# Performance work log

Measured on AMD Instinct MI355X. Metric: run time of the kernel, lower is better.

## Reference

```python
import jax, jax.numpy as jnp
import numpy as np
import math

DIM = 4096
N_HEADS = 32
HEAD_DIM = DIM // N_HEADS  # 128
SEQLEN = 2048


def setup_inputs() -> dict:
    key = jax.random.key(0)
    ks = jax.random.split(key, 8)
    x = jax.random.normal(ks[0], (1, SEQLEN, DIM), dtype=jnp.float32)
    # freqs_cis as real view: (seqlen, head_dim//2, 2) = (cos, sin) of rotary angles
    theta = 10000.0 ** (-jnp.arange(0, HEAD_DIM, 2, dtype=jnp.float32) / HEAD_DIM)
    angles = jnp.arange(SEQLEN, dtype=jnp.float32)[:, None] * theta[None, :]
    freqs = jnp.stack([jnp.cos(angles), jnp.sin(angles)], axis=-1)  # (S, 64, 2)
    # causal additive mask (use -1e9 instead of -inf for numeric safety)
    mask = jnp.triu(jnp.full((SEQLEN, SEQLEN), -1e9, dtype=jnp.float32), k=1)[None, None]
    scale = 1.0 / math.sqrt(DIM)
    wq = jax.random.normal(ks[1], (DIM, DIM), dtype=jnp.float32) * scale
    wk = jax.random.normal(ks[2], (DIM, DIM), dtype=jnp.float32) * scale
    wv = jax.random.normal(ks[3], (DIM, DIM), dtype=jnp.float32) * scale
    wo = jax.random.normal(ks[4], (DIM, DIM), dtype=jnp.float32) * scale
    return {"x": x, "start_pos": 0, "freqs": freqs, "mask": mask,
            "wq": wq, "wk": wk, "wv": wv, "wo": wo}


def _rotary(xq, xk, freqs, seqlen, n_heads, head_dim):
    # Faithful to source: note the repo's slice(0, 2) means xq_ == xq (no pair swap).
    ll = freqs[:, :, 0:1]  # (S, hd/2, 1) cos
    rr = freqs[:, :, 1:2]  # (S, hd/2, 1) sin
    fl = jnp.concatenate([ll, ll], axis=-1).reshape(seqlen, 1, head_dim)
    fr = jnp.concatenate([-rr, rr], axis=-1).reshape(seqlen, 1, head_dim)
    xq_ = xq.reshape(seqlen, n_heads, head_dim // 2, 2).reshape(seqlen, n_heads, head_dim)  # == xq
    xk_ = xk.reshape(seqlen, n_heads, head_dim // 2, 2).reshape(seqlen, n_heads, head_dim)  # == xk
    return xq * fl + xq_ * fr, xk * fl + xk_ * fr


def reference(x, start_pos, freqs, mask, wq, wk, wv, wo):
    bsz, seqlen, dim = x.shape  # bsz == 1 (source squeezes batch)
    xs = x[0]  # (S, D) -- HE encrypt/linear/decrypt roundtrip == plain linear
    xq = xs @ wq.T
    xk = xs @ wk.T
    xv = xs @ wv.T
    xq = xq.reshape(seqlen, N_HEADS, HEAD_DIM)
    xk = xk.reshape(seqlen, N_HEADS, HEAD_DIM)
    xv = xv.reshape(seqlen, N_HEADS, HEAD_DIM)
    xq, xk = _rotary(xq, xk, freqs, seqlen, N_HEADS, HEAD_DIM)
    # start_pos == 0 and zero-initialized cache => keys/values are just xk/xv
    q = jnp.transpose(xq, (1, 0, 2))  # (H, S, Dh)
    k = jnp.transpose(xk, (1, 0, 2))
    v = jnp.transpose(xv, (1, 0, 2))
    scores = jnp.einsum('hqd,hkd->hqk', q, k) / math.sqrt(HEAD_DIM)  # (H, S, S)
    scores = scores[None] + mask  # (1, H, S, S)
    probs = jax.nn.softmax(scores, axis=-1)
    out = jnp.einsum('bhqk,hkd->bhqd', probs, v)  # (1, H, S, Dh)
    out = jnp.transpose(out, (0, 2, 1, 3)).reshape(bsz, seqlen, dim)
    return out @ wo.T
```

## Files before the change

kernel.cpp:

```cpp
#include <hip/hip_runtime.h>

#define DIM 4096
#define SEQ 2048
#define NH 32
#define HD 128

typedef __bf16 bf16x8 __attribute__((ext_vector_type(8)));
typedef float f32x4 __attribute__((ext_vector_type(4)));

#define QSCALE 0.12751649736765598f

__device__ inline ushort f2bf(float f) {
    union { float f; unsigned u; } v; v.f = f;
    unsigned r = v.u + 0x7fffu + ((v.u >> 16) & 1u);
    return (ushort)(r >> 16);
}

__global__ void conv_all(const float* __restrict__ x,  const float* __restrict__ wq,
                         const float* __restrict__ wk, const float* __restrict__ wv,
                         const float* __restrict__ wo,
                         ushort* __restrict__ xb,  ushort* __restrict__ wqb,
                         ushort* __restrict__ wkb, ushort* __restrict__ wvb,
                         ushort* __restrict__ wob) {
    int i = blockIdx.x * 256 + threadIdx.x;
    const float* src; ushort* dst; int off;
    const int n4x = (SEQ * DIM) / 4;
    if (i < n4x) { src = x; dst = xb; off = i; }
    else {
        int j = i - n4x;
        int w = j >> 22;
        off = j & ((1 << 22) - 1);
        src = (w == 0) ? wq : (w == 1) ? wk : (w == 2) ? wv : wo;
        dst = (w == 0) ? wqb : (w == 1) ? wkb : (w == 2) ? wvb : wob;
    }
    float4 v = ((const float4*)src)[off];
    ushort4 o;
    o.x = f2bf(v.x); o.y = f2bf(v.y); o.z = f2bf(v.z); o.w = f2bf(v.w);
    ((ushort4*)dst)[off] = o;
}


#define AS1(p) (const __attribute__((address_space(1))) void*)(p)
#define AS3(p) (__attribute__((address_space(3))) void*)(p)
#define FENCE() asm volatile("" ::: "memory")
#define BARRIER() do { FENCE(); __builtin_amdgcn_s_barrier(); FENCE(); } while (0)

__device__ __forceinline__ void gemm256_body(
    const ushort* __restrict__ Ab,
    const ushort* __restrict__ Bb,
    ushort* __restrict__ sA0, ushort* __restrict__ sA1,
    ushort* __restrict__ sB0, ushort* __restrict__ sB1,
    f32x4 acc[8][4], const int ldk, const int klen)
{
    const int tid  = threadIdx.x;
    const int wave = tid >> 6, lane = tid & 63;
    const int quad = lane >> 4, c = lane & 15;
    const int wm = wave >> 2, wn = wave & 3;

    const int aoff  = (lane >> 3) * ldk + (((lane & 7) ^ (lane >> 3)) * 8);
    const int sa_r0 = wave * 8;
    const int sb_r0 = (wave >> 1) * 64 + (wave & 1) * 16;

    const int rp0 = (quad ^ (c & 7)) * 8;
    const int rp1 = ((4 + quad) ^ (c & 7)) * 8;
    const int arow = (wm * 128 + c) * 64;
    const int brow = (wn * 64 + c) * 64;

#define STAGE_A(dst, h, k0) do { \
    const int _r0 = (h) * 64 + sa_r0; \
    __builtin_amdgcn_global_load_lds(AS1(Ab + (size_t)_r0 * ldk + (k0) + aoff), \
                                     AS3((dst) + _r0 * 64), 16, 0, 0); \
    const int _r1 = _r0 + 128; \
    __builtin_amdgcn_global_load_lds(AS1(Ab + (size_t)_r1 * ldk + (k0) + aoff), \
                                     AS3((dst) + _r1 * 64), 16, 0, 0); \
  } while (0)
#define STAGE_B(dst, h, k0) do { \
    const int _r0 = (h) * 32 + sb_r0; \
    __builtin_amdgcn_global_load_lds(AS1(Bb + (size_t)_r0 * ldk + (k0) + aoff), \
                                     AS3((dst) + _r0 * 64), 16, 0, 0); \
    const int _r1 = _r0 + 8; \
    __builtin_amdgcn_global_load_lds(AS1(Bb + (size_t)_r1 * ldk + (k0) + aoff), \
                                     AS3((dst) + _r1 * 64), 16, 0, 0); \
  } while (0)

    bf16x8 af[4][2];
    bf16x8 b0[2][2];
    bf16x8 b1[2][2];

#define READ_AH(buf, mh) do { \
    _Pragma("unroll") \
    for (int _m = 0; _m < 4; ++_m) { \
        af[_m][0] = *(const bf16x8*)&(buf)[arow + (mh) * 4096 + _m * 1024 + rp0]; \
        af[_m][1] = *(const bf16x8*)&(buf)[arow + (mh) * 4096 + _m * 1024 + rp1]; \
    } } while (0)
#define READ_BH(buf, nh, dst) do { \
    _Pragma("unroll") \
    for (int _n = 0; _n < 2; ++_n) { \
        dst[_n][0] = *(const bf16x8*)&(buf)[brow + (nh) * 2048 + _n * 1024 + rp0]; \
        dst[_n][1] = *(const bf16x8*)&(buf)[brow + (nh) * 2048 + _n * 1024 + rp1]; \
    } } while (0)
#define MMA_Q(mh, nq, B) do { \
    __builtin_amdgcn_s_setprio(1); \
    _Pragma("unroll") \
    for (int _kk = 0; _kk < 2; ++_kk) \
    _Pragma("unroll") \
    for (int _m = 0; _m < 4; ++_m) \
    _Pragma("unroll") \
    for (int _n = 0; _n < 2; ++_n) \
        acc[(mh) * 4 + _m][(nq) * 2 + _n] = __builtin_amdgcn_mfma_f32_16x16x32_bf16( \
            af[_m][_kk], B[_n][_kk], acc[(mh) * 4 + _m][(nq) * 2 + _n], 0, 0, 0); \
    __builtin_amdgcn_s_setprio(0); \
  } while (0)

    const int NT = klen >> 6;

    STAGE_B(sB0, 0, 0);  STAGE_A(sA0, 0, 0);
    STAGE_B(sB0, 1, 0);  STAGE_A(sA0, 1, 0);
    STAGE_B(sB1, 0, 64); STAGE_A(sA1, 0, 64);
    STAGE_B(sB1, 1, 64); STAGE_A(sA1, 1, 64);
    asm volatile("s_waitcnt vmcnt(8)" ::: "memory");
    BARRIER();
    READ_BH(sB0, 0, b0);
    BARRIER();

#pragma unroll 1
    for (int t = 0; t < NT; ++t) {
        ushort* cA = (t & 1) ? sA1 : sA0;
        ushort* cB = (t & 1) ? sB1 : sB0;
        ushort* nB = (t & 1) ? sB0 : sB1;
        const int kn2 = (t + 2) << 6;
        const bool ok1 = (t + 1 < NT), ok2 = (t + 2 < NT);

        READ_AH(cA, 0);
        if (ok2) STAGE_B(cB, 0, kn2);
        BARRIER();
        MMA_Q(0, 0, b0);
        BARRIER();

        READ_BH(cB, 1, b1);
        if (ok2) STAGE_A(cA, 0, kn2);
        BARRIER();
        MMA_Q(0, 1, b1);
        BARRIER();

        READ_AH(cA, 1);
        if (ok2) STAGE_B(cB, 1, kn2);
        BARRIER();
        MMA_Q(1, 1, b1);
        BARRIER();

        if (ok1) {
            if (ok2) asm volatile("s_waitcnt vmcnt(6)" ::: "memory");
            else     asm volatile("s_waitcnt vmcnt(0)" ::: "memory");
            BARRIER();
            if (ok2) STAGE_A(cA, 1, kn2);
        }
        BARRIER();
        MMA_Q(1, 0, b0);
        if (ok1) READ_BH(nB, 0, b0);
        BARRIER();
    }
#undef STAGE_A
#undef STAGE_B
#undef READ_AH
#undef READ_BH
#undef MMA_Q
}

__global__ __launch_bounds__(512, 2)
void gemm_qkv(const ushort* __restrict__ A,
              const ushort* __restrict__ Bq, const ushort* __restrict__ Bk,
              const ushort* __restrict__ Bv,
              ushort* __restrict__ qout, ushort* __restrict__ kout,
              ushort* __restrict__ vt, const float* __restrict__ freqs) {
    __shared__ __align__(16) ushort sA[2][256 * 64];
    __shared__ __align__(16) ushort sB[2][256 * 64];
    const int bi = blockIdx.x;
    const int x = bi & 7;
    const int l = bi >> 3;
    const int mblk = l & 7;
    const int nblk = x * 6 + (l >> 3);
    const int wsel = nblk >> 4;
    const int nloc = (nblk & 15) * 256;
    const int m0 = mblk * 256;
    const ushort* B = (wsel == 0) ? Bq : (wsel == 1) ? Bk : Bv;

    const f32x4 vzero = {0.f, 0.f, 0.f, 0.f};
    f32x4 acc[8][4];
#pragma unroll
    for (int i = 0; i < 8; i++)
#pragma unroll
        for (int j = 0; j < 4; j++) acc[i][j] = vzero;

    gemm256_body(A + (size_t)m0 * DIM, B + (size_t)nloc * DIM,
                 &sA[0][0], &sA[1][0], &sB[0][0], &sB[1][0], acc, DIM, DIM);

    const int tid = threadIdx.x;
    const int wave = tid >> 6, lane = tid & 63;
    const int quad = lane >> 4, c = lane & 15;
    const int wm = wave >> 2, wn = wave & 3;

    if (wsel < 2) {
        ushort* Cw = wsel ? kout : qout;
        const float qs = wsel ? 1.0f : QSCALE;
#pragma unroll
        for (int i = 0; i < 8; i++) {
#pragma unroll
            for (int j = 0; j < 4; j++) {
                int colg = nloc + wn * 64 + j * 16 + c;
                int dh = (colg & 127) >> 1;
#pragma unroll
                for (int r = 0; r < 4; r++) {
                    int row = m0 + wm * 128 + i * 16 + quad * 4 + r;
                    float2 f2 = ((const float2*)freqs)[row * 64 + dh];
                    float f = (f2.x + ((c & 1) ? f2.y : -f2.y)) * qs;
                    Cw[(size_t)row * DIM + colg] = f2bf(acc[i][j][r] * f);
                }
            }
        }
    } else {
#pragma unroll
        for (int i = 0; i < 8; i++) {
#pragma unroll
            for (int j = 0; j < 4; j++) {
                int cv = nloc + wn * 64 + j * 16 + c;
                int row0 = m0 + wm * 128 + i * 16 + quad * 4;
                ushort4 o;
                o.x = f2bf(acc[i][j][0]); o.y = f2bf(acc[i][j][1]);
                o.z = f2bf(acc[i][j][2]); o.w = f2bf(acc[i][j][3]);
                *(ushort4*)&vt[(size_t)cv * SEQ + row0] = o;
            }
        }
    }
}

__global__ __launch_bounds__(512, 2)
void gemm_f32out(const ushort* __restrict__ A, const ushort* __restrict__ B,
                 float* __restrict__ C, float* __restrict__ P,
                 int M, int N, int K) {
    __shared__ __align__(16) ushort sA[2][256 * 64];
    __shared__ __align__(16) ushort sB[2][256 * 64];
    const int bi = blockIdx.x;
    const int kh = bi >> 7;
    const int r  = bi & 127;
    const int x = r & 7;
    const int l = r >> 3;
    const int mblk = l & 7;
    const int nblk = x * 2 + (l >> 3);
    const int m0 = mblk * 256, n0 = nblk * 256;
    const int khalf = K >> 1;

    const f32x4 vzero = {0.f, 0.f, 0.f, 0.f};
    f32x4 acc[8][4];
#pragma unroll
    for (int i = 0; i < 8; i++)
#pragma unroll
        for (int j = 0; j < 4; j++) acc[i][j] = vzero;

    gemm256_body(A + (size_t)m0 * K + kh * khalf, B + (size_t)n0 * K + kh * khalf,
                 &sA[0][0], &sA[1][0], &sB[0][0], &sB[1][0], acc, K, khalf);

    const int tid = threadIdx.x;
    const int wave = tid >> 6, lane = tid & 63;
    const int quad = lane >> 4, c = lane & 15;
    const int wm = wave >> 2, wn = wave & 3;
    float* dst = kh ? P : C;

#pragma unroll
    for (int i = 0; i < 8; i++)
#pragma unroll
        for (int j = 0; j < 4; j++)
#pragma unroll
            for (int r2 = 0; r2 < 4; r2++) {
                int row = m0 + wm * 128 + i * 16 + quad * 4 + r2;
                int col = n0 + wn * 64 + j * 16 + c;
                dst[(size_t)row * N + col] = acc[i][j][r2];
            }
}

__global__ void add_partial(float* __restrict__ C, const float* __restrict__ P) {
    int i = blockIdx.x * 256 + threadIdx.x;
    float4 a = ((const float4*)C)[i];
    float4 b = ((const float4*)P)[i];
    a.x += b.x; a.y += b.y; a.z += b.z; a.w += b.w;
    ((float4*)C)[i] = a;
}

__global__ __launch_bounds__(256)
void flash_kernel(const ushort* __restrict__ Q, const ushort* __restrict__ K,
                  const ushort* __restrict__ Vt, ushort* __restrict__ O) {
    const int bi = blockIdx.x;
    const int h = bi & (NH - 1);
    const int p = bi >> 5;
    __shared__ __align__(16) ushort sK[2][64 * 128];
    __shared__ __align__(16) ushort sVt[2][128 * 64];
    __shared__ __align__(16) ushort sP[4][16 * 72];
    const int tid = threadIdx.x, wave = tid >> 6, lane = tid & 63;
    const int quad = lane >> 4, c = lane & 15;

#define STAGE_KV(db, kt) do { \
    _Pragma("unroll") \
    for (int _i = 0; _i < 4; _i++) { \
        int _lr = wave * 16 + _i * 4 + (lane >> 4); \
        int _ch = lane & 15; \
        int _g = (_ch & 8) | ((_ch ^ _lr) & 7); \
        __builtin_amdgcn_global_load_lds( \
            AS1(K + (size_t)((kt) * 64 + _lr) * DIM + h * HD + _g * 8), \
            AS3(&sK[db][(wave * 16 + _i * 4) * 128]), 16, 0, 0); \
    } \
    _Pragma("unroll") \
    for (int _i = 0; _i < 4; _i++) { \
        int _ld = wave * 32 + _i * 8 + (lane >> 3); \
        int _ch = lane & 7; \
        int _g = (_ch ^ _ld) & 7; \
        __builtin_amdgcn_global_load_lds( \
            AS1(Vt + (size_t)(h * HD + _ld) * SEQ + (kt) * 64 + _g * 8), \
            AS3(&sVt[db][(wave * 32 + _i * 8) * 64]), 16, 0, 0); \
    } } while (0)

    for (int pass = 0; pass < 2; pass++) {
        const int qb = pass ? (SEQ / 64 - 1 - p) : p;
        const int q0 = qb * 64;

        bf16x8 qf[4];
        {
            const ushort* Qp = Q + (size_t)(q0 + wave * 16 + c) * DIM + h * HD;
#pragma unroll
            for (int ks = 0; ks < 4; ks++) qf[ks] = *(const bf16x8*)(Qp + ks * 32 + quad * 8);
        }
        const f32x4 vzero = {0.f, 0.f, 0.f, 0.f};
        f32x4 oa[8];
#pragma unroll
        for (int dt = 0; dt < 8; dt++) oa[dt] = vzero;
        float ms[4], ls[4];
#pragma unroll
        for (int r = 0; r < 4; r++) { ms[r] = -1e30f; ls[r] = 0.f; }

        STAGE_KV(0, 0);

#pragma unroll 1
        for (int kt = 0; kt <= qb; kt++) {
            const int b = kt & 1;
            if (kt < qb) {
                STAGE_KV(b ^ 1, kt + 1);
                asm volatile("s_waitcnt vmcnt(8)" ::: "memory");
            } else {
                asm volatile("s_waitcnt vmcnt(0)" ::: "memory");
            }
            BARRIER();

            f32x4 s[4];
#pragma unroll
            for (int nt = 0; nt < 4; nt++) s[nt] = vzero;
            __builtin_amdgcn_s_setprio(1);
#pragma unroll
            for (int ks = 0; ks < 4; ks++)
#pragma unroll
                for (int nt = 0; nt < 4; nt++) {
                    int lr = nt * 16 + c;
                    int gc = ks * 4 + quad;
                    int pch = (gc & 8) | ((gc ^ lr) & 7);
                    bf16x8 kf = *(const bf16x8*)&sK[b][lr * 128 + pch * 8];
                    s[nt] = __builtin_amdgcn_mfma_f32_16x16x32_bf16(qf[ks], kf, s[nt], 0, 0, 0);
                }
            __builtin_amdgcn_s_setprio(0);

            if (kt == qb) {
#pragma unroll
                for (int nt = 0; nt < 4; nt++)
#pragma unroll
                    for (int r = 0; r < 4; r++) {
                        int keyg = nt * 16 + c;
                        int qg   = wave * 16 + quad * 4 + r;
                        if (keyg > qg) s[nt][r] = -1e30f;
                    }
            }

            float mnew[4], alpha[4];
#pragma unroll
            for (int r = 0; r < 4; r++) {
                float v = fmaxf(fmaxf(s[0][r], s[1][r]), fmaxf(s[2][r], s[3][r]));
                v = fmaxf(v, __shfl_xor(v, 1));
                v = fmaxf(v, __shfl_xor(v, 2));
                v = fmaxf(v, __shfl_xor(v, 4));
                v = fmaxf(v, __shfl_xor(v, 8));
                mnew[r]  = fmaxf(ms[r], v);
                alpha[r] = exp2f(ms[r] - mnew[r]);
                ms[r]    = mnew[r];
            }
            float rs[4] = {0.f, 0.f, 0.f, 0.f};
#pragma unroll
            for (int nt = 0; nt < 4; nt++)
#pragma unroll
                for (int r = 0; r < 4; r++) {
                    float pv = exp2f(s[nt][r] - mnew[r]);
                    rs[r] += pv;
                    sP[wave][(quad * 4 + r) * 72 + nt * 16 + c] = f2bf(pv);
                }
#pragma unroll
            for (int r = 0; r < 4; r++) {
                float v = rs[r];
                v += __shfl_xor(v, 1);
                v += __shfl_xor(v, 2);
                v += __shfl_xor(v, 4);
                v += __shfl_xor(v, 8);
                ls[r] = ls[r] * alpha[r] + v;
            }
#pragma unroll
            for (int dt = 0; dt < 8; dt++)
#pragma unroll
                for (int r = 0; r < 4; r++) oa[dt][r] *= alpha[r];

            __asm__ volatile("s_waitcnt lgkmcnt(0)" ::: "memory");

            __builtin_amdgcn_s_setprio(1);
#pragma unroll
            for (int k2 = 0; k2 < 2; k2++) {
                bf16x8 pf = *(const bf16x8*)&sP[wave][c * 72 + k2 * 32 + quad * 8];
#pragma unroll
                for (int dt = 0; dt < 8; dt++) {
                    int ld = dt * 16 + c;
                    int gc = k2 * 4 + quad;
                    int pch = (gc ^ ld) & 7;
                    bf16x8 vf = *(const bf16x8*)&sVt[b][ld * 64 + pch * 8];
                    oa[dt] = __builtin_amdgcn_mfma_f32_16x16x32_bf16(pf, vf, oa[dt], 0, 0, 0);
                }
            }
            __builtin_amdgcn_s_setprio(0);

            BARRIER();
        }

#pragma unroll
        for (int r = 0; r < 4; r++) {
            float inv = 1.f / ls[r];
            int row = q0 + wave * 16 + quad * 4 + r;
#pragma unroll
            for (int dt = 0; dt < 8; dt++)
                O[(size_t)row * DIM + h * HD + dt * 16 + c] = f2bf(oa[dt][r] * inv);
        }
    }
#undef STAGE_KV
}

extern "C" void kernel_launch(void* const* d_in, const int* in_sizes, int n_in,
                              void* d_out, int out_size, void* d_ws, size_t ws_size,
                              hipStream_t stream) {
    const float* x     = (const float*)d_in[0];
    const float* freqs = (const float*)d_in[2];
    const float* wq    = (const float*)d_in[4];
    const float* wk    = (const float*)d_in[5];
    const float* wv    = (const float*)d_in[6];
    const float* wo    = (const float*)d_in[7];
    float* out = (float*)d_out;

    ushort* xb    = (ushort*)d_ws;
    ushort* wqb   = xb    + (size_t)SEQ * DIM;
    ushort* wkb   = wqb   + (size_t)DIM * DIM;
    ushort* wvb   = wkb   + (size_t)DIM * DIM;
    ushort* wob   = wvb   + (size_t)DIM * DIM;
    ushort* qbuf  = wob   + (size_t)DIM * DIM;
    ushort* kbuf  = qbuf  + (size_t)SEQ * DIM;
    ushort* vtbuf = kbuf  + (size_t)SEQ * DIM;
    ushort* obuf  = vtbuf + (size_t)SEQ * DIM;
    float* pbuf = (float*)wqb;

    const int n4tot = (SEQ * DIM + 4 * DIM * DIM) / 4;
    conv_all<<<n4tot / 256, 256, 0, stream>>>(x, wq, wk, wv, wo, xb, wqb, wkb, wvb, wob);

    gemm_qkv<<<dim3(384), 512, 0, stream>>>(xb, wqb, wkb, wvb, qbuf, kbuf, vtbuf, freqs);

    flash_kernel<<<dim3(NH * SEQ / 128), 256, 0, stream>>>(qbuf, kbuf, vtbuf, obuf);

    gemm_f32out<<<dim3(256), 512, 0, stream>>>(obuf, wob, out, pbuf, SEQ, DIM, DIM);
    add_partial<<<dim3(SEQ * DIM / 4 / 256), 256, 0, stream>>>(out, pbuf);
}
```

Measured before the change: 697.5 us.

## Process 128-row query tiles per flash block with two row groups per wave

The flash attention kernel now assigns each block a single 128-row query tile, with each wave holding two 16-row groups, instead of two paired 64-row tiles per block. This halves K/V tile staging per query row and shares each staged K/V tile across more MFMA work. It also adds a launch-bounds occupancy hint of 2 blocks. The price is unbalanced causal work: blocks now run between 2 and 32 KV tiles each, where before every block did the same amount via the balanced pairing. Per-row-group causal skipping adds branching inside the loop.

```diff
diff --git a/kernel.cpp b/kernel.cpp
--- a/kernel.cpp
+++ b/kernel.cpp
@@ -286,12 +286,15 @@
     ((float4*)C)[i] = a;
 }
 
-__global__ __launch_bounds__(256)
+__global__ __launch_bounds__(256, 2)
 void flash_kernel(const ushort* __restrict__ Q, const ushort* __restrict__ K,
                   const ushort* __restrict__ Vt, ushort* __restrict__ O) {
     const int bi = blockIdx.x;
     const int h = bi & (NH - 1);
-    const int p = bi >> 5;
+    const int t = bi >> 5;
+    const int qb = (t < 8) ? t : 23 - t;
+    const int q0 = qb * 128;
+    const int NT = 2 * qb + 2;
     __shared__ __align__(16) ushort sK[2][64 * 128];
     __shared__ __align__(16) ushort sVt[2][128 * 64];
     __shared__ __align__(16) ushort sP[4][16 * 72];
@@ -318,128 +321,136 @@
             AS3(&sVt[db][(wave * 32 + _i * 8) * 64]), 16, 0, 0); \
     } } while (0)
 
-    for (int pass = 0; pass < 2; pass++) {
-        const int qb = pass ? (SEQ / 64 - 1 - p) : p;
-        const int q0 = qb * 64;
-
-        bf16x8 qf[4];
-        {
-            const ushort* Qp = Q + (size_t)(q0 + wave * 16 + c) * DIM + h * HD;
-#pragma unroll
-            for (int ks = 0; ks < 4; ks++) qf[ks] = *(const bf16x8*)(Qp + ks * 32 + quad * 8);
-        }
-        const f32x4 vzero = {0.f, 0.f, 0.f, 0.f};
-        f32x4 oa[8];
-#pragma unroll
-        for (int dt = 0; dt < 8; dt++) oa[dt] = vzero;
-        float ms[4], ls[4];
-#pragma unroll
-        for (int r = 0; r < 4; r++) { ms[r] = -1e30f; ls[r] = 0.f; }
-
-        STAGE_KV(0, 0);
+    bf16x8 qf[2][4];
+#pragma unroll
+    for (int rg = 0; rg < 2; rg++) {
+        const ushort* Qp = Q + (size_t)(q0 + wave * 32 + rg * 16 + c) * DIM + h * HD;
+#pragma unroll
+        for (int ks = 0; ks < 4; ks++) qf[rg][ks] = *(const bf16x8*)(Qp + ks * 32 + quad * 8);
+    }
+    const f32x4 vzero = {0.f, 0.f, 0.f, 0.f};
+    f32x4 oa[2][8];
+#pragma unroll
+    for (int rg = 0; rg < 2; rg++)
+#pragma unroll
+        for (int dt = 0; dt < 8; dt++) oa[rg][dt] = vzero;
+    float ms[2][4], ls[2][4];
+#pragma unroll
+    for (int rg = 0; rg < 2; rg++)
+#pragma unroll
+        for (int r = 0; r < 4; r++) { ms[rg][r] = -1e30f; ls[rg][r] = 0.f; }
+
+    STAGE_KV(0, 0);
 
 #pragma unroll 1
-        for (int kt = 0; kt <= qb; kt++) {
-            const int b = kt & 1;
-            if (kt < qb) {
-                STAGE_KV(b ^ 1, kt + 1);
-                asm volatile("s_waitcnt vmcnt(8)" ::: "memory");
-            } else {
-                asm volatile("s_waitcnt vmcnt(0)" ::: "memory");
+    for (int kt = 0; kt < NT; kt++) {
+        const int b = kt & 1;
+        if (kt + 1 < NT) {
+            STAGE_KV(b ^ 1, kt + 1);
+            asm volatile("s_waitcnt vmcnt(8)" ::: "memory");
+        } else {
+            asm volatile("s_waitcnt vmcnt(0)" ::: "memory");
+        }
+        BARRIER();
+
+#pragma unroll
+        for (int rg = 0; rg < 2; rg++) {
+            const int rowlo = q0 + wave * 32 + rg * 16;
+            if (kt * 64 <= rowlo + 15) {
+                f32x4 s[4];
+#pragma unroll
+                for (int nt = 0; nt < 4; nt++) s[nt] = vzero;
+                __builtin_amdgcn_s_setprio(1);
+#pragma unroll
+                for (int ks = 0; ks < 4; ks++)
+#pragma unroll
+                    for (int nt = 0; nt < 4; nt++) {
+                        int lr = nt * 16 + c;
+                        int gc = ks * 4 + quad;
+                        int pch = (gc & 8) | ((gc ^ lr) & 7);
+                        bf16x8 kf = *(const bf16x8*)&sK[b][lr * 128 + pch * 8];
+                        s[nt] = __builtin_amdgcn_mfma_f32_16x16x32_bf16(qf[rg][ks], kf, s[nt], 0, 0, 0);
+                    }
+                __builtin_amdgcn_s_setprio(0);
+
+                if (kt >= 2 * qb) {
+#pragma unroll
+                    for (int nt = 0; nt < 4; nt++)
+#pragma unroll
+                        for (int r = 0; r < 4; r++) {
+                            int keyg = kt * 64 + nt * 16 + c;
+                            int qg   = rowlo + quad * 4 + r;
+                            if (keyg > qg) s[nt][r] = -1e30f;
+                        }
+                }
+
+                float mnew[4], alpha[4];
+#pragma unroll
+                for (int r = 0; r < 4; r++) {
+                    float v = fmaxf(fmaxf(s[0][r], s[1][r]), fmaxf(s[2][r], s[3][r]));
+                    v = fmaxf(v, __shfl_xor(v, 1));
+                    v = fmaxf(v, __shfl_xor(v, 2));
+                    v = fmaxf(v, __shfl_xor(v, 4));
+                    v = fmaxf(v, __shfl_xor(v, 8));
+                    mnew[r]   = fmaxf(ms[rg][r], v);
+                    alpha[r]  = exp2f(ms[rg][r] - mnew[r]);
+                    ms[rg][r] = mnew[r];
+                }
+                float rs[4] = {0.f, 0.f, 0.f, 0.f};
+#pragma unroll
+                for (int nt = 0; nt < 4; nt++)
+#pragma unroll
+                    for (int r = 0; r < 4; r++) {
+                        float pv = exp2f(s[nt][r] - mnew[r]);
+                        rs[r] += pv;
+                        sP[wave][(quad * 4 + r) * 72 + nt * 16 + c] = f2bf(pv);
+                    }
+#pragma unroll
+                for (int r = 0; r < 4; r++) {
+                    float v = rs[r];
+                    v += __shfl_xor(v, 1);
+                    v += __shfl_xor(v, 2);
+                    v += __shfl_xor(v, 4);
+                    v += __shfl_xor(v, 8);
+                    ls[rg][r] = ls[rg][r] * alpha[r] + v;
+                }
+#pragma unroll
+                for (int dt = 0; dt < 8; dt++)
+#pragma unroll
+                    for (int r = 0; r < 4; r++) oa[rg][dt][r] *= alpha[r];
+
+                __asm__ volatile("s_waitcnt lgkmcnt(0)" ::: "memory");
+
+                __builtin_amdgcn_s_setprio(1);
+#pragma unroll
+                for (int k2 = 0; k2 < 2; k2++) {
+                    bf16x8 pf = *(const bf16x8*)&sP[wave][c * 72 + k2 * 32 + quad * 8];
+#pragma unroll
+                    for (int dt = 0; dt < 8; dt++) {
+                        int ld = dt * 16 + c;
+                        int gc = k2 * 4 + quad;
+                        int pch = (gc ^ ld) & 7;
+                        bf16x8 vf = *(const bf16x8*)&sVt[b][ld * 64 + pch * 8];
+                        oa[rg][dt] = __builtin_amdgcn_mfma_f32_16x16x32_bf16(pf, vf, oa[rg][dt], 0, 0, 0);
+                    }
+                }
+                __builtin_amdgcn_s_setprio(0);
             }
-            BARRIER();
-
-            f32x4 s[4];
-#pragma unroll
-            for (int nt = 0; nt < 4; nt++) s[nt] = vzero;
-            __builtin_amdgcn_s_setprio(1);
-#pragma unroll
-            for (int ks = 0; ks < 4; ks++)
-#pragma unroll
-                for (int nt = 0; nt < 4; nt++) {
-                    int lr = nt * 16 + c;
-                    int gc = ks * 4 + quad;
-                    int pch = (gc & 8) | ((gc ^ lr) & 7);
-                    bf16x8 kf = *(const bf16x8*)&sK[b][lr * 128 + pch * 8];
-                    s[nt] = __builtin_amdgcn_mfma_f32_16x16x32_bf16(qf[ks], kf, s[nt], 0, 0, 0);
-                }
-            __builtin_amdgcn_s_setprio(0);
-
-            if (kt == qb) {
-#pragma unroll
-                for (int nt = 0; nt < 4; nt++)
-#pragma unroll
-                    for (int r = 0; r < 4; r++) {
-                        int keyg = nt * 16 + c;
-                        int qg   = wave * 16 + quad * 4 + r;
-                        if (keyg > qg) s[nt][r] = -1e30f;
-                    }
-            }
-
-            float mnew[4], alpha[4];
-#pragma unroll
-            for (int r = 0; r < 4; r++) {
-                float v = fmaxf(fmaxf(s[0][r], s[1][r]), fmaxf(s[2][r], s[3][r]));
-                v = fmaxf(v, __shfl_xor(v, 1));
-                v = fmaxf(v, __shfl_xor(v, 2));
-                v = fmaxf(v, __shfl_xor(v, 4));
-                v = fmaxf(v, __shfl_xor(v, 8));
-                mnew[r]  = fmaxf(ms[r], v);
-                alpha[r] = exp2f(ms[r] - mnew[r]);
-                ms[r]    = mnew[r];
-            }
-            float rs[4] = {0.f, 0.f, 0.f, 0.f};
-#pragma unroll
-            for (int nt = 0; nt < 4; nt++)
-#pragma unroll
-                for (int r = 0; r < 4; r++) {
-                    float pv = exp2f(s[nt][r] - mnew[r]);
-                    rs[r] += pv;
-                    sP[wave][(quad * 4 + r) * 72 + nt * 16 + c] = f2bf(pv);
-                }
-#pragma unroll
-            for (int r = 0; r < 4; r++) {
-                float v = rs[r];
-                v += __shfl_xor(v, 1);
-                v += __shfl_xor(v, 2);
-                v += __shfl_xor(v, 4);
-                v += __shfl_xor(v, 8);
-                ls[r] = ls[r] * alpha[r] + v;
-            }
+        }
+
+        BARRIER();
+    }
+
+#pragma unroll
+    for (int rg = 0; rg < 2; rg++)
+#pragma unroll
+        for (int r = 0; r < 4; r++) {
+            float inv = 1.f / ls[rg][r];
+            int row = q0 + wave * 32 + rg * 16 + quad * 4 + r;
 #pragma unroll
             for (int dt = 0; dt < 8; dt++)
-#pragma unroll
-                for (int r = 0; r < 4; r++) oa[dt][r] *= alpha[r];
-
-            __asm__ volatile("s_waitcnt lgkmcnt(0)" ::: "memory");
-
-            __builtin_amdgcn_s_setprio(1);
-#pragma unroll
-            for (int k2 = 0; k2 < 2; k2++) {
-                bf16x8 pf = *(const bf16x8*)&sP[wave][c * 72 + k2 * 32 + quad * 8];
-#pragma unroll
-                for (int dt = 0; dt < 8; dt++) {
-                    int ld = dt * 16 + c;
-                    int gc = k2 * 4 + quad;
-                    int pch = (gc ^ ld) & 7;
-                    bf16x8 vf = *(const bf16x8*)&sVt[b][ld * 64 + pch * 8];
-                    oa[dt] = __builtin_amdgcn_mfma_f32_16x16x32_bf16(pf, vf, oa[dt], 0, 0, 0);
-                }
-            }
-            __builtin_amdgcn_s_setprio(0);
-
-            BARRIER();
-        }
-
-#pragma unroll
-        for (int r = 0; r < 4; r++) {
-            float inv = 1.f / ls[r];
-            int row = q0 + wave * 16 + quad * 4 + r;
-#pragma unroll
-            for (int dt = 0; dt < 8; dt++)
-                O[(size_t)row * DIM + h * HD + dt * 16 + c] = f2bf(oa[dt][r] * inv);
-        }
-    }
+                O[(size_t)row * DIM + h * HD + dt * 16 + c] = f2bf(oa[rg][dt][r] * inv);
+        }
 #undef STAGE_KV
 }
 
@@ -470,7 +481,7 @@
 
     gemm_qkv<<<dim3(384), 512, 0, stream>>>(xb, wqb, wkb, wvb, qbuf, kbuf, vtbuf, freqs);
 
-    flash_kernel<<<dim3(NH * SEQ / 128), 256, 0, stream>>>(qbuf, kbuf, vtbuf, obuf);
+    flash_kernel<<<dim3(512), 256, 0, stream>>>(qbuf, kbuf, vtbuf, obuf);
 
     gemm_f32out<<<dim3(256), 512, 0, stream>>>(obuf, wob, out, pbuf, SEQ, DIM, DIM);
     add_partial<<<dim3(SEQ * DIM / 4 / 256), 256, 0, stream>>>(out, pbuf);
```

Measured after the change: 735.8 us. 5.5% more time.

## Load K and V fragments directly from global memory in flash attention

Applied to the files above, without the earlier changes.

Drops the double-buffered LDS staging of K and Vt tiles, along with the per-tile barriers. Each wave now reads its MFMA operand fragments straight from global memory and relies on the L1/L2 caches for reuse across the four waves. Launch bounds add a minimum of 2 blocks per SM, which frees LDS for higher occupancy. The cost is redundant global traffic, since every wave reloads the same K/V, and the loss of the latency hiding the prefetch provided. The grid size is rewritten as the literal 512, which equals the old expression.

```diff
diff --git a/kernel.cpp b/kernel.cpp
--- a/kernel.cpp
+++ b/kernel.cpp
@@ -286,37 +286,18 @@
     ((float4*)C)[i] = a;
 }
 
-__global__ __launch_bounds__(256)
+__global__ __launch_bounds__(256, 2)
 void flash_kernel(const ushort* __restrict__ Q, const ushort* __restrict__ K,
                   const ushort* __restrict__ Vt, ushort* __restrict__ O) {
     const int bi = blockIdx.x;
     const int h = bi & (NH - 1);
     const int p = bi >> 5;
-    __shared__ __align__(16) ushort sK[2][64 * 128];
-    __shared__ __align__(16) ushort sVt[2][128 * 64];
     __shared__ __align__(16) ushort sP[4][16 * 72];
     const int tid = threadIdx.x, wave = tid >> 6, lane = tid & 63;
     const int quad = lane >> 4, c = lane & 15;
 
-#define STAGE_KV(db, kt) do { \
-    _Pragma("unroll") \
-    for (int _i = 0; _i < 4; _i++) { \
-        int _lr = wave * 16 + _i * 4 + (lane >> 4); \
-        int _ch = lane & 15; \
-        int _g = (_ch & 8) | ((_ch ^ _lr) & 7); \
-        __builtin_amdgcn_global_load_lds( \
-            AS1(K + (size_t)((kt) * 64 + _lr) * DIM + h * HD + _g * 8), \
-            AS3(&sK[db][(wave * 16 + _i * 4) * 128]), 16, 0, 0); \
-    } \
-    _Pragma("unroll") \
-    for (int _i = 0; _i < 4; _i++) { \
-        int _ld = wave * 32 + _i * 8 + (lane >> 3); \
-        int _ch = lane & 7; \
-        int _g = (_ch ^ _ld) & 7; \
-        __builtin_amdgcn_global_load_lds( \
-            AS1(Vt + (size_t)(h * HD + _ld) * SEQ + (kt) * 64 + _g * 8), \
-            AS3(&sVt[db][(wave * 32 + _i * 8) * 64]), 16, 0, 0); \
-    } } while (0)
+    const ushort* Kp = K + (size_t)c * DIM + h * HD + quad * 8;
+    const ushort* Vp = Vt + (size_t)(h * HD + c) * SEQ + quad * 8;
 
     for (int pass = 0; pass < 2; pass++) {
         const int qb = pass ? (SEQ / 64 - 1 - p) : p;
@@ -336,19 +317,9 @@
 #pragma unroll
         for (int r = 0; r < 4; r++) { ms[r] = -1e30f; ls[r] = 0.f; }
 
-        STAGE_KV(0, 0);
-
 #pragma unroll 1
         for (int kt = 0; kt <= qb; kt++) {
-            const int b = kt & 1;
-            if (kt < qb) {
-                STAGE_KV(b ^ 1, kt + 1);
-                asm volatile("s_waitcnt vmcnt(8)" ::: "memory");
-            } else {
-                asm volatile("s_waitcnt vmcnt(0)" ::: "memory");
-            }
-            BARRIER();
-
+            const ushort* Kt = Kp + (size_t)kt * 64 * DIM;
             f32x4 s[4];
 #pragma unroll
             for (int nt = 0; nt < 4; nt++) s[nt] = vzero;
@@ -357,10 +328,7 @@
             for (int ks = 0; ks < 4; ks++)
 #pragma unroll
                 for (int nt = 0; nt < 4; nt++) {
-                    int lr = nt * 16 + c;
-                    int gc = ks * 4 + quad;
-                    int pch = (gc & 8) | ((gc ^ lr) & 7);
-                    bf16x8 kf = *(const bf16x8*)&sK[b][lr * 128 + pch * 8];
+                    bf16x8 kf = *(const bf16x8*)(Kt + (size_t)nt * 16 * DIM + ks * 32);
                     s[nt] = __builtin_amdgcn_mfma_f32_16x16x32_bf16(qf[ks], kf, s[nt], 0, 0, 0);
                 }
             __builtin_amdgcn_s_setprio(0);
@@ -413,22 +381,18 @@
 
             __asm__ volatile("s_waitcnt lgkmcnt(0)" ::: "memory");
 
+            const ushort* Vtk = Vp + kt * 64;
             __builtin_amdgcn_s_setprio(1);
 #pragma unroll
             for (int k2 = 0; k2 < 2; k2++) {
                 bf16x8 pf = *(const bf16x8*)&sP[wave][c * 72 + k2 * 32 + quad * 8];
 #pragma unroll
                 for (int dt = 0; dt < 8; dt++) {
-                    int ld = dt * 16 + c;
-                    int gc = k2 * 4 + quad;
-                    int pch = (gc ^ ld) & 7;
-                    bf16x8 vf = *(const bf16x8*)&sVt[b][ld * 64 + pch * 8];
+                    bf16x8 vf = *(const bf16x8*)(Vtk + (size_t)dt * 16 * SEQ + k2 * 32);
                     oa[dt] = __builtin_amdgcn_mfma_f32_16x16x32_bf16(pf, vf, oa[dt], 0, 0, 0);
                 }
             }
             __builtin_amdgcn_s_setprio(0);
-
-            BARRIER();
         }
 
 #pragma unroll
@@ -440,7 +404,6 @@
                 O[(size_t)row * DIM + h * HD + dt * 16 + c] = f2bf(oa[dt][r] * inv);
         }
     }
-#undef STAGE_KV
 }
 
 extern "C" void kernel_launch(void* const* d_in, const int* in_sizes, int n_in,
@@ -470,7 +433,7 @@
 
     gemm_qkv<<<dim3(384), 512, 0, stream>>>(xb, wqb, wkb, wvb, qbuf, kbuf, vtbuf, freqs);
 
-    flash_kernel<<<dim3(NH * SEQ / 128), 256, 0, stream>>>(qbuf, kbuf, vtbuf, obuf);
+    flash_kernel<<<dim3(512), 256, 0, stream>>>(qbuf, kbuf, vtbuf, obuf);
 
     gemm_f32out<<<dim3(256), 512, 0, stream>>>(obuf, wob, out, pbuf, SEQ, DIM, DIM);
     add_partial<<<dim3(SEQ * DIM / 4 / 256), 256, 0, stream>>>(out, pbuf);
```

New measurement: 881.3 us. 1.26x slower.
